# Kernel optimization log

Measured on AMD Instinct MI355X. Metric: run time of the kernel, lower is better.

## Reference

```python
import jax, jax.numpy as jnp
import numpy as np

# Config matching init_kwargs
N_SEGMENT = 8
N_GROUP = 8
K = 3            # correlation_neighbor
PAD = K // 2     # 1
BN_EPS = 1e-5


def setup_inputs() -> dict:
    key = jax.random.key(0)
    k1, k2, k3 = jax.random.split(key, 3)
    nt, c, h, w = 64, 256, 56, 56
    x = jax.random.normal(k1, (nt, c, h, w), dtype=jnp.float32)
    # Conv2d(72 -> 144, groups=8, kernel=1): weight [144, 9, 1, 1], bias [144]
    w_conv = jax.random.normal(k2, (144, 9, 1, 1), dtype=jnp.float32) * 0.1
    b_conv = jax.random.normal(k3, (144,), dtype=jnp.float32) * 0.1
    gamma = jnp.ones((c,), dtype=jnp.float32)
    beta = jnp.zeros((c,), dtype=jnp.float32)
    return {"x": x, "w_conv": w_conv, "b_conv": b_conv, "gamma": gamma, "beta": beta}


def reference(x, w_conv, b_conv, gamma, beta):
    nt, c, h, w = x.shape
    G = N_GROUP
    cg = c // G
    nt2 = nt // 2

    # ReplicationPad2d(1)
    xp = jnp.pad(x, ((0, 0), (0, 0), (PAD, PAD), (PAD, PAD)), mode="edge")
    x_even = x[::2]          # [nt2, c, h, w]
    xp_odd = xp[1::2]        # [nt2, c, h+2, w+2]

    # Cost volume: shifted multiply + per-group channel sum, 3x3 offsets
    corrs = []
    for i in range(K):
        for j in range(K):
            corr = x_even * jax.lax.slice(xp_odd, (0, 0, i, j), (nt2, c, i + h, j + w))
            corr = corr.reshape(nt2, G, cg, h, w).sum(axis=2)  # [nt2, G, h, w]
            corrs.append(corr)
    corr_feat = jnp.stack(corrs, axis=1)  # [nt2, 9, G, h, w] (offset outer, group inner)

    # Grouped 1x1 conv (groups=G): contiguous channel split of the [9*G] layout
    cr = corr_feat.reshape(nt2, G, K * K, h, w)               # [nt2, G, 9, h, w]
    wg = w_conv.reshape(G, 2 * K * K, K * K)                  # [G, 18, 9]
    xcorr = jnp.einsum("ngihw,goi->ngohw", cr, wg) + b_conv.reshape(1, G, 2 * K * K, 1, 1)
    # view(nt2, 3, 3, 2*G, h, w)
    xcorr = xcorr.reshape(nt2, K, K, 2 * G, h, w)

    # x_pad viewed as (nt, c_per_group, n_group, H+2, W+2)  (group is inner here!)
    xp2 = xp.reshape(nt, cg, G, h + 2, w + 2)
    xp_e = xp2[::2]   # even frames [nt2, cg, G, h+2, w+2]
    xp_o = xp2[1::2]  # odd frames

    # Weighted re-fusion over the 9 offsets (accumulate to avoid a big stack)
    acc = jnp.zeros((nt2, cg, G, h, w), dtype=x.dtype)
    for i in range(K):
        for j in range(K):
            we = xcorr[:, i, j, 0::2][:, None]  # [nt2, 1, G, h, w]
            wo = xcorr[:, i, j, 1::2][:, None]
            acc = acc + xp_e[:, :, :, i:i + h, j:j + w] * we \
                      + xp_o[:, :, :, i:i + h, j:j + w] * wo
    out = acc.reshape(nt2, c, h, w)  # (cg outer, G inner) flatten matches torch view

    # BatchNorm2d (training-mode batch statistics)
    mean = out.mean(axis=(0, 2, 3), keepdims=True)
    var = out.var(axis=(0, 2, 3), keepdims=True)
    out = (out - mean) * jax.lax.rsqrt(var + BN_EPS)
    out = out * gamma.reshape(1, c, 1, 1) + beta.reshape(1, c, 1, 1)
    return out
```

## Files before the change

kernel.cpp:

```cpp
#include <hip/hip_runtime.h>
#include <cstdint>

#define HW 3136
#define WID 56
#define NBLK 1792

__device__ __forceinline__ int clampi(int v, int lo, int hi) {
    return v < lo ? lo : (v > hi ? hi : v);
}

__global__ __launch_bounds__(256, 2) void tf_fused(
    const float* __restrict__ x, const float* __restrict__ wconv,
    const float* __restrict__ bconv, float* __restrict__ out)
{
    __shared__ float CR[72 * 56];
    __shared__ float CP[4 * 9 * 56];

    const int d = blockIdx.x;
    const int logical = (d & 7) * 224 + (d >> 3);
    const int n  = logical / 56;
    const int r0 = logical % 56;
    const int t = threadIdx.x;
    const int su = __builtin_amdgcn_readfirstlane(t >> 6);
    const int lane = t & 63;
    const bool act = lane < WID;
    const int px = act ? lane : (WID - 1);

    const float* xe = x + (size_t)(2 * n) * 256 * HW;
    const float* xo = xe + (size_t)256 * HW;

    const int cbm = clampi(px - 1, 0, 55);
    const int cbp = px < 55 ? px + 1 : 55;
    int rb[3];
    #pragma unroll
    for (int di = 0; di < 3; ++di) rb[di] = clampi(r0 + di - 1, 0, 55) * WID;
    const int rc = r0 * WID + px;

    #pragma unroll
    for (int g = 0; g < 8; ++g) {
        float crg[9];
        #pragma unroll
        for (int i = 0; i < 9; ++i) crg[i] = 0.f;

        #pragma unroll
        for (int sub = 0; sub < 4; ++sub) {
            const int ch0 = (4 * g + sub) * 8 + 2 * su;
            const float* pe = xe + (size_t)ch0 * HW;
            const float* po = xo + (size_t)ch0 * HW;
            const float e0 = pe[rc];
            const float e1 = pe[HW + rc];
            #pragma unroll
            for (int di = 0; di < 3; ++di) {
                #pragma unroll
                for (int dj = 0; dj < 3; ++dj) {
                    const int cc = (dj == 0) ? cbm : ((dj == 1) ? px : cbp);
                    const float o0 = po[rb[di] + cc];
                    const float o1 = po[HW + rb[di] + cc];
                    crg[di * 3 + dj] += e0 * o0 + e1 * o1;
                }
            }
        }
        if (act) {
            #pragma unroll
            for (int ij = 0; ij < 9; ++ij)
                CP[(su * 9 + ij) * 56 + px] = crg[ij];
        }
        __syncthreads();
        #pragma unroll
        for (int ij = su; ij < 9; ij += 4) {
            if (act) {
                const float v = CP[(0 * 9 + ij) * 56 + px]
                              + CP[(1 * 9 + ij) * 56 + px]
                              + CP[(2 * 9 + ij) * 56 + px]
                              + CP[(3 * 9 + ij) * 56 + px];
                CR[(ij * 8 + g) * 56 + px] = v;
            }
        }
        __syncthreads();
    }

    float Wv[9][4];
    #pragma unroll
    for (int ij = 0; ij < 9; ++ij)
        #pragma unroll
        for (int j = 0; j < 4; ++j) {
            const int f = ij * 16 + 4 * su + j;
            const int a = f / 18;
            float w = bconv[f];
            #pragma unroll
            for (int b = 0; b < 9; ++b)
                w += CR[(a * 9 + b) * 56 + px] * wconv[f * 9 + b];
            Wv[ij][j] = w;
        }

    float* ob = out + (size_t)n * 256 * HW + r0 * WID;

    for (int q = 0; q < 32; ++q) {
        const int ch = q * 8 + 2 * su;
        const float* pe = xe + (size_t)ch * HW;
        const float* po = xo + (size_t)ch * HW;

        float a0 = 0.f, a1 = 0.f;
        #pragma unroll
        for (int di = 0; di < 3; ++di) {
            #pragma unroll
            for (int dj = 0; dj < 3; ++dj) {
                const int ij = di * 3 + dj;
                const int cc = (dj == 0) ? cbm : ((dj == 1) ? px : cbp);
                const float ev0 = pe[rb[di] + cc];
                const float ev1 = pe[HW + rb[di] + cc];
                const float ov0 = po[rb[di] + cc];
                const float ov1 = po[HW + rb[di] + cc];
                a0 += ev0 * Wv[ij][0] + ov0 * Wv[ij][1];
                a1 += ev1 * Wv[ij][2] + ov1 * Wv[ij][3];
            }
        }
        if (act) {
            ob[(size_t)ch * HW + lane] = a0;
            ob[(size_t)(ch + 1) * HW + lane] = a1;
        }
    }
}

__global__ void tf_stats_part(const float* __restrict__ out,
                              float* __restrict__ ps, float* __restrict__ pq)
{
    const int ch = blockIdx.x >> 3;
    const int sl = blockIdx.x & 7;
    const int t = threadIdx.x;

    float s = 0.f, q = 0.f;
    #pragma unroll
    for (int k = 0; k < 4; ++k) {
        const float4* p = (const float4*)(out + ((size_t)(4 * sl + k) * 256 + ch) * HW);
        for (int i = t; i < 784; i += 256) {
            const float4 v = p[i];
            s += v.x + v.y + v.z + v.w;
            q += v.x * v.x + v.y * v.y + v.z * v.z + v.w * v.w;
        }
    }
    #pragma unroll
    for (int o = 32; o >= 1; o >>= 1) {
        s += __shfl_xor(s, o);
        q += __shfl_xor(q, o);
    }
    __shared__ float rs[4], rq[4];
    if ((t & 63) == 0) { rs[t >> 6] = s; rq[t >> 6] = q; }
    __syncthreads();
    if (t == 0) {
        ps[blockIdx.x] = rs[0] + rs[1] + rs[2] + rs[3];
        pq[blockIdx.x] = rq[0] + rq[1] + rq[2] + rq[3];
    }
}

__global__ void tf_stats_fin(const float* __restrict__ ps, const float* __restrict__ pq,
                             const float* __restrict__ gamma, const float* __restrict__ beta,
                             float* __restrict__ AB)
{
    const int ch = threadIdx.x;
    float s = 0.f, q = 0.f;
    #pragma unroll
    for (int sl = 0; sl < 8; ++sl) {
        s += ps[ch * 8 + sl];
        q += pq[ch * 8 + sl];
    }
    const float inv = 1.f / 100352.f;
    const float mean = s * inv;
    const float var = q * inv - mean * mean;
    const float rstd = rsqrtf(var + 1e-5f);
    const float A = gamma[ch] * rstd;
    AB[ch] = A;
    AB[256 + ch] = beta[ch] - mean * A;
}

__global__ void tf_norm(float* __restrict__ out, const float* __restrict__ AB)
{
    const unsigned total4 = 32u * 256u * 784u;
    unsigned i = blockIdx.x * 256u + threadIdx.x;
    const unsigned stride = gridDim.x * 256u;
    float4* o4 = (float4*)out;
    for (; i < total4; i += stride) {
        const unsigned ch = (i / 784u) & 255u;
        const float A = AB[ch], B = AB[256 + ch];
        float4 v = o4[i];
        v.x = v.x * A + B;
        v.y = v.y * A + B;
        v.z = v.z * A + B;
        v.w = v.w * A + B;
        o4[i] = v;
    }
}

extern "C" void kernel_launch(void* const* d_in, const int* in_sizes, int n_in,
                              void* d_out, int out_size, void* d_ws, size_t ws_size,
                              hipStream_t stream) {
    const float* x     = (const float*)d_in[0];
    const float* wconv = (const float*)d_in[1];
    const float* bconv = (const float*)d_in[2];
    const float* gamma = (const float*)d_in[3];
    const float* beta  = (const float*)d_in[4];
    float* out = (float*)d_out;

    float* ps = (float*)d_ws;
    float* pq = ps + 2048;
    float* AB = pq + 2048;

    tf_fused<<<NBLK, 256, 0, stream>>>(x, wconv, bconv, out);
    tf_stats_part<<<2048, 256, 0, stream>>>(out, ps, pq);
    tf_stats_fin<<<1, 256, 0, stream>>>(ps, pq, gamma, beta, AB);
    tf_norm<<<2048, 256, 0, stream>>>(out, AB);
}
```

Before: 196.9 us.

## Vectorize fused kernel to float4 pixels with bpermute-based horizontal taps

Each thread now handles four adjacent pixels, loaded as float4. Horizontal neighbours for the 3x3 taps come from ds_bpermute across lanes, replacing separate scalar clamped loads. Work is split over 16 channel-pair slices per block, and the cross-slice reduction is done in two LDS passes with float4 partial sums. This cuts global load instruction count and redundant neighbour loads, at the cost of lane shuffles, extra syncs per group, and two idle lanes out of every 16.

```diff
diff --git a/kernel.cpp b/kernel.cpp
--- a/kernel.cpp
+++ b/kernel.cpp
@@ -9,117 +9,155 @@
     return v < lo ? lo : (v > hi ? hi : v);
 }
 
+__device__ __forceinline__ float bperm(int a4, float v) {
+    return __int_as_float(__builtin_amdgcn_ds_bpermute(a4, __float_as_int(v)));
+}
+
+__device__ __forceinline__ void fma4(float4& a, const float4& u, const float4& w) {
+    a.x += u.x * w.x; a.y += u.y * w.y; a.z += u.z * w.z; a.w += u.w * w.w;
+}
+
 __global__ __launch_bounds__(256, 2) void tf_fused(
     const float* __restrict__ x, const float* __restrict__ wconv,
     const float* __restrict__ bconv, float* __restrict__ out)
 {
-    __shared__ float CR[72 * 56];
-    __shared__ float CP[4 * 9 * 56];
+    __shared__ float4 CP[16 * 5 * 14];
+    __shared__ float  CR[72 * 56];
 
     const int d = blockIdx.x;
     const int logical = (d & 7) * 224 + (d >> 3);
     const int n  = logical / 56;
     const int r0 = logical % 56;
     const int t = threadIdx.x;
-    const int su = __builtin_amdgcn_readfirstlane(t >> 6);
-    const int lane = t & 63;
-    const bool act = lane < WID;
-    const int px = act ? lane : (WID - 1);
+    const int wv = t >> 6;
+    const int l = t & 63;
+    const int qd0 = l & 15;
+    const int s16 = wv * 4 + (l >> 4);
+    const bool act = qd0 < 14;
+    const int qd = act ? qd0 : 13;
+    const int gl = s16 & 7;
 
     const float* xe = x + (size_t)(2 * n) * 256 * HW;
     const float* xo = xe + (size_t)256 * HW;
 
-    const int cbm = clampi(px - 1, 0, 55);
-    const int cbp = px < 55 ? px + 1 : 55;
+    const int am = ((qd0 == 0) ? l : (l - 1)) * 4;
+    const int ap = ((qd0 >= 13) ? l : (l + 1)) * 4;
+    const bool le = (qd0 == 0);
+    const bool re = (qd0 >= 13);
+
     int rb[3];
     #pragma unroll
-    for (int di = 0; di < 3; ++di) rb[di] = clampi(r0 + di - 1, 0, 55) * WID;
-    const int rc = r0 * WID + px;
-
-    #pragma unroll
+    for (int di = 0; di < 3; ++di) rb[di] = clampi(r0 + di - 1, 0, 55) * WID + qd * 4;
+    const int rc = r0 * WID + qd * 4;
+
+#define MKTAPS(v, Tm, Tp)                                   \
+    {                                                       \
+        const float lwp = bperm(am, (v).w);                 \
+        const float rwp = bperm(ap, (v).x);                 \
+        const float lw = le ? (v).x : lwp;                  \
+        const float rw = re ? (v).w : rwp;                  \
+        Tm = make_float4(lw, (v).x, (v).y, (v).z);          \
+        Tp = make_float4((v).y, (v).z, (v).w, rw);          \
+    }
+
     for (int g = 0; g < 8; ++g) {
-        float crg[9];
-        #pragma unroll
-        for (int i = 0; i < 9; ++i) crg[i] = 0.f;
-
-        #pragma unroll
-        for (int sub = 0; sub < 4; ++sub) {
-            const int ch0 = (4 * g + sub) * 8 + 2 * su;
-            const float* pe = xe + (size_t)ch0 * HW;
-            const float* po = xo + (size_t)ch0 * HW;
-            const float e0 = pe[rc];
-            const float e1 = pe[HW + rc];
-            #pragma unroll
-            for (int di = 0; di < 3; ++di) {
-                #pragma unroll
-                for (int dj = 0; dj < 3; ++dj) {
-                    const int cc = (dj == 0) ? cbm : ((dj == 1) ? px : cbp);
-                    const float o0 = po[rb[di] + cc];
-                    const float o1 = po[HW + rb[di] + cc];
-                    crg[di * 3 + dj] += e0 * o0 + e1 * o1;
-                }
+        const int ch0 = g * 32 + 2 * s16;
+        const float* pe = xe + (size_t)ch0 * HW;
+        const float* po = xo + (size_t)ch0 * HW;
+        const float4 E0 = *(const float4*)(pe + rc);
+        const float4 E1 = *(const float4*)(pe + HW + rc);
+
+        float4 crg[9];
+        #pragma unroll
+        for (int i = 0; i < 9; ++i) crg[i] = make_float4(0.f, 0.f, 0.f, 0.f);
+
+        #pragma unroll
+        for (int di = 0; di < 3; ++di) {
+            const float4 O0 = *(const float4*)(po + rb[di]);
+            const float4 O1 = *(const float4*)(po + HW + rb[di]);
+            float4 T0m, T0p, T1m, T1p;
+            MKTAPS(O0, T0m, T0p)
+            MKTAPS(O1, T1m, T1p)
+            fma4(crg[di * 3 + 0], E0, T0m); fma4(crg[di * 3 + 0], E1, T1m);
+            fma4(crg[di * 3 + 1], E0, O0);  fma4(crg[di * 3 + 1], E1, O1);
+            fma4(crg[di * 3 + 2], E0, T0p); fma4(crg[di * 3 + 2], E1, T1p);
+        }
+
+        if (act) {
+            #pragma unroll
+            for (int ij = 0; ij < 5; ++ij) CP[(s16 * 5 + ij) * 14 + qd] = crg[ij];
+        }
+        __syncthreads();
+        if (t < 70) {
+            const int ij = t / 14, qu = t % 14;
+            float4 s = CP[ij * 14 + qu];
+            #pragma unroll
+            for (int sl = 1; sl < 16; ++sl) {
+                const float4 v = CP[(sl * 5 + ij) * 14 + qu];
+                s.x += v.x; s.y += v.y; s.z += v.z; s.w += v.w;
             }
-        }
+            *(float4*)(CR + (ij * 8 + g) * 56 + qu * 4) = s;
+        }
+        __syncthreads();
         if (act) {
             #pragma unroll
-            for (int ij = 0; ij < 9; ++ij)
-                CP[(su * 9 + ij) * 56 + px] = crg[ij];
-        }
-        __syncthreads();
-        #pragma unroll
-        for (int ij = su; ij < 9; ij += 4) {
-            if (act) {
-                const float v = CP[(0 * 9 + ij) * 56 + px]
-                              + CP[(1 * 9 + ij) * 56 + px]
-                              + CP[(2 * 9 + ij) * 56 + px]
-                              + CP[(3 * 9 + ij) * 56 + px];
-                CR[(ij * 8 + g) * 56 + px] = v;
+            for (int ij = 5; ij < 9; ++ij) CP[(s16 * 5 + ij - 5) * 14 + qd] = crg[ij];
+        }
+        __syncthreads();
+        if (t < 56) {
+            const int ij = 5 + t / 14, qu = t % 14;
+            float4 s = CP[(ij - 5) * 14 + qu];
+            #pragma unroll
+            for (int sl = 1; sl < 16; ++sl) {
+                const float4 v = CP[(sl * 5 + ij - 5) * 14 + qu];
+                s.x += v.x; s.y += v.y; s.z += v.z; s.w += v.w;
             }
-        }
-        __syncthreads();
-    }
-
-    float Wv[9][4];
-    #pragma unroll
-    for (int ij = 0; ij < 9; ++ij)
-        #pragma unroll
-        for (int j = 0; j < 4; ++j) {
-            const int f = ij * 16 + 4 * su + j;
-            const int a = f / 18;
-            float w = bconv[f];
-            #pragma unroll
-            for (int b = 0; b < 9; ++b)
-                w += CR[(a * 9 + b) * 56 + px] * wconv[f * 9 + b];
-            Wv[ij][j] = w;
-        }
-
-    float* ob = out + (size_t)n * 256 * HW + r0 * WID;
-
-    for (int q = 0; q < 32; ++q) {
-        const int ch = q * 8 + 2 * su;
+            *(float4*)(CR + (ij * 8 + g) * 56 + qu * 4) = s;
+        }
+        __syncthreads();
+    }
+
+    float4 We[9], Wo[9];
+    #pragma unroll
+    for (int ij = 0; ij < 9; ++ij) {
+        const int fe = ij * 16 + 2 * gl;
+        const int a = fe / 18;
+        const float be = bconv[fe], bo = bconv[fe + 1];
+        float4 we = make_float4(be, be, be, be);
+        float4 wo = make_float4(bo, bo, bo, bo);
+        #pragma unroll
+        for (int b = 0; b < 9; ++b) {
+            const float4 c4 = *(const float4*)(CR + (a * 9 + b) * 56 + qd * 4);
+            const float wce = wconv[fe * 9 + b];
+            const float wco = wconv[fe * 9 + 9 + b];
+            we.x += c4.x * wce; we.y += c4.y * wce; we.z += c4.z * wce; we.w += c4.w * wce;
+            wo.x += c4.x * wco; wo.y += c4.y * wco; wo.z += c4.z * wco; wo.w += c4.w * wco;
+        }
+        We[ij] = we; Wo[ij] = wo;
+    }
+
+    float* ob = out + (size_t)n * 256 * HW + r0 * WID + qd * 4;
+
+    for (int k = 0; k < 16; ++k) {
+        const int ch = k * 16 + s16;
         const float* pe = xe + (size_t)ch * HW;
         const float* po = xo + (size_t)ch * HW;
 
-        float a0 = 0.f, a1 = 0.f;
+        float4 acc = make_float4(0.f, 0.f, 0.f, 0.f);
         #pragma unroll
         for (int di = 0; di < 3; ++di) {
-            #pragma unroll
-            for (int dj = 0; dj < 3; ++dj) {
-                const int ij = di * 3 + dj;
-                const int cc = (dj == 0) ? cbm : ((dj == 1) ? px : cbp);
-                const float ev0 = pe[rb[di] + cc];
-                const float ev1 = pe[HW + rb[di] + cc];
-                const float ov0 = po[rb[di] + cc];
-                const float ov1 = po[HW + rb[di] + cc];
-                a0 += ev0 * Wv[ij][0] + ov0 * Wv[ij][1];
-                a1 += ev1 * Wv[ij][2] + ov1 * Wv[ij][3];
-            }
-        }
-        if (act) {
-            ob[(size_t)ch * HW + lane] = a0;
-            ob[(size_t)(ch + 1) * HW + lane] = a1;
-        }
-    }
+            const float4 E = *(const float4*)(pe + rb[di]);
+            const float4 O = *(const float4*)(po + rb[di]);
+            float4 TEm, TEp, TOm, TOp;
+            MKTAPS(E, TEm, TEp)
+            MKTAPS(O, TOm, TOp)
+            fma4(acc, TEm, We[di * 3 + 0]); fma4(acc, TOm, Wo[di * 3 + 0]);
+            fma4(acc, E,   We[di * 3 + 1]); fma4(acc, O,   Wo[di * 3 + 1]);
+            fma4(acc, TEp, We[di * 3 + 2]); fma4(acc, TOp, Wo[di * 3 + 2]);
+        }
+        if (act) *(float4*)(ob + (size_t)ch * HW) = acc;
+    }
+#undef MKTAPS
 }
 
 __global__ void tf_stats_part(const float* __restrict__ out,
```

After: 229.5 us. +16.6%, slower.
